# Kernel tuning notes

Measured on AMD Instinct MI355X. Metric: run time of the kernel, lower is better.

## Reference

```python
import jax, jax.numpy as jnp
import numpy as np

L, D, H, E, EH, K = 3, 1024, 16, 8, 256, 2
HD = D // H
B, S, DIN, NOUT = 2, 1024, 32, 8
BASE = 10000.0
EPS = 1e-5


def _ln(x, g, b):
    m = jnp.mean(x, -1, keepdims=True)
    v = jnp.mean((x - m) ** 2, -1, keepdims=True)
    return (x - m) * jax.lax.rsqrt(v + EPS) * g + b


def _rope_tables():
    inv = 1.0 / (BASE ** (jnp.arange(0, HD, 2, dtype=jnp.float32) / HD))
    f = jnp.arange(S, dtype=jnp.float32)[:, None] * inv[None, :]  # [S, HD/2]
    emb = jnp.concatenate([f, f], -1)  # [S, HD]
    return jnp.cos(emb), jnp.sin(emb)


def _rot_half(x):
    x1, x2 = jnp.split(x, 2, axis=-1)
    return jnp.concatenate([-x2, x1], -1)


def setup_inputs() -> dict:
    key = jax.random.key(0)
    ks = iter(jax.random.split(key, 40))
    n = lambda shp, s=0.02: jax.random.normal(next(ks), shp, jnp.float32) * s
    return dict(
        x=jax.random.normal(next(ks), (B, S, DIN), jnp.float32),
        ln1_g=jnp.ones((L, D)), ln1_b=jnp.zeros((L, D)),
        qw=n((L, D, D)), qb=jnp.zeros((L, D)),
        kw=n((L, D, D)), kb=jnp.zeros((L, D)),
        vw=n((L, D, D)), vb=jnp.zeros((L, D)),
        ow=n((L, D, D)), ob=jnp.zeros((L, D)),
        ln2_g=jnp.ones((L, D)), ln2_b=jnp.zeros((L, D)),
        sel_w=n((L, D, E)),
        w1=n((L, E, D, EH)), w2=n((L, E, EH, D)),
        lnf_t_g=jnp.ones((D,)), lnf_t_b=jnp.zeros((D,)),
        lnf_d_g=jnp.ones((D,)), lnf_d_b=jnp.zeros((D,)),
        in_w=n((D, DIN)), in_b=jnp.zeros((D,)),
        out_w=n((NOUT, D)), out_b=jnp.zeros((NOUT,)),
    )


def reference(x, ln1_g, ln1_b, qw, qb, kw, kb, vw, vb, ow, ob, ln2_g, ln2_b,
              sel_w, w1, w2, lnf_t_g, lnf_t_b, lnf_d_g, lnf_d_b,
              in_w, in_b, out_w, out_b):
    cos, sin = _rope_tables()
    scale = HD ** -0.5
    # input projection (torch Linear: x @ W.T + b)
    h = jnp.einsum('bti,di->btd', x, in_w) + in_b

    def layer(h, p):
        l1g, l1b, qw_, qb_, kw_, kb_, vw_, vb_, ow_, ob_, l2g, l2b, selw, w1_, w2_ = p
        xn = _ln(h, l1g, l1b)
        # torch uses F.linear(x, W.t()) => y = x @ W
        def heads(y):
            return y.reshape(B, S, H, HD).transpose(0, 2, 1, 3)
        q = heads(xn @ qw_ + qb_)
        k = heads(xn @ kw_ + kb_)
        v = heads(xn @ vw_ + vb_)
        q = q * cos + _rot_half(q) * sin
        k = k * cos + _rot_half(k) * sin
        attn = jax.nn.softmax(jnp.einsum('bhsd,bhtd->bhst', q, k) * scale, axis=-1)
        o = jnp.einsum('bhst,bhtd->bhsd', attn, v).transpose(0, 2, 1, 3).reshape(B, S, D)
        h = h + jnp.einsum('bsd,od->bso', o, ow_) + ob_
        # SigmaMoE: sigmoid gate, top-k experts, relu FFN experts
        xn = _ln(h, l2g, l2b)
        gates = jax.nn.sigmoid(xn @ selw)  # [B,S,E]
        topv, topi = jax.lax.top_k(gates, K)
        m = jnp.sum(jax.nn.one_hot(topi, E, dtype=xn.dtype) * topv[..., None], axis=-2)  # [B,S,E]
        mid = jax.nn.relu(jnp.einsum('bsd,edh->bseh', xn, w1_))
        moe = jnp.einsum('bseh,ehd->bsd', mid * m[..., None], w2_)
        return h + moe, None

    params = (ln1_g, ln1_b, qw, qb, kw, kb, vw, vb, ow, ob, ln2_g, ln2_b, sel_w, w1, w2)
    h, _ = jax.lax.scan(layer, h, params)
    h = _ln(h, lnf_t_g, lnf_t_b)           # transformer final LN
    last = _ln(h[:, -1, :], lnf_d_g, lnf_d_b)  # decoder LN on last token
    return last @ out_w.T + out_b  # [B, NOUT]
```

## Files before the change

### kernel.cpp

```cpp
#include <hip/hip_runtime.h>


#define LNUM 3
#define D 1024
#define H 16
#define HD 64
#define E 8
#define EH 256
#define B 2
#define S 1024
#define DIN 32
#define NOUT 8
#define EPS 1e-5f
#define TOK (B * S)

typedef __bf16 bf16x8 __attribute__((ext_vector_type(8)));
typedef __bf16 bf16x4 __attribute__((ext_vector_type(4)));
typedef float fx4 __attribute__((ext_vector_type(4)));

__device__ inline float block_reduce_sum256(float v, float* scratch) {
  int lane = threadIdx.x & 63, wv = threadIdx.x >> 6;
#pragma unroll
  for (int off = 32; off; off >>= 1) v += __shfl_down(v, off);
  __syncthreads();
  if (lane == 0) scratch[wv] = v;
  __syncthreads();
  return scratch[0] + scratch[1] + scratch[2] + scratch[3];
}

__global__ __launch_bounds__(256) void ln_bf_kernel(
    const float* __restrict__ in, const float* __restrict__ g,
    const float* __restrict__ bta, __bf16* __restrict__ outb) {
  int token = blockIdx.x;
  int tid = threadIdx.x;
  const float* p = in + (size_t)token * D;
  __shared__ float scratch[4];
  float x[4];
  float s = 0.f, sq = 0.f;
#pragma unroll
  for (int i = 0; i < 4; i++) {
    x[i] = p[tid + i * 256];
    s += x[i];
    sq += x[i] * x[i];
  }
  s = block_reduce_sum256(s, scratch);
  sq = block_reduce_sum256(sq, scratch);
  float mean = s * (1.f / D);
  float inv = rsqrtf(sq * (1.f / D) - mean * mean + EPS);
  __bf16* obp = outb + (size_t)token * D;
#pragma unroll
  for (int i = 0; i < 4; i++) {
    int d = tid + i * 256;
    obp[d] = (__bf16)((x[i] - mean) * inv * g[d] + bta[d]);
  }
}

__global__ __launch_bounds__(256) void ln_gate_kernel(
    const float* __restrict__ in, const float* __restrict__ g,
    const float* __restrict__ bta, const float* __restrict__ selw,
    __bf16* __restrict__ outb, float* __restrict__ gm) {
  int token = blockIdx.x;
  int tid = threadIdx.x;
  const float* p = in + (size_t)token * D;
  __shared__ float scratch[4];
  float x[4];
  float s = 0.f, sq = 0.f;
#pragma unroll
  for (int i = 0; i < 4; i++) {
    x[i] = p[tid + i * 256];
    s += x[i];
    sq += x[i] * x[i];
  }
  s = block_reduce_sum256(s, scratch);
  sq = block_reduce_sum256(sq, scratch);
  float mean = s * (1.f / D);
  float inv = rsqrtf(sq * (1.f / D) - mean * mean + EPS);
  __bf16* obp = outb + (size_t)token * D;
  float ge[E];
#pragma unroll
  for (int e = 0; e < E; e++) ge[e] = 0.f;
#pragma unroll
  for (int i = 0; i < 4; i++) {
    int d = tid + i * 256;
    float y = (x[i] - mean) * inv * g[d] + bta[d];
    obp[d] = (__bf16)y;
#pragma unroll
    for (int e = 0; e < E; e++) ge[e] += y * selw[d * E + e];
  }
  __shared__ float red[4][E];
  int lane = tid & 63, wv = tid >> 6;
#pragma unroll
  for (int e = 0; e < E; e++) {
    float vv = ge[e];
#pragma unroll
    for (int off = 32; off; off >>= 1) vv += __shfl_down(vv, off);
    if (lane == 0) red[wv][e] = vv;
  }
  __syncthreads();
  if (tid == 0) {
    float gg[E];
    for (int e = 0; e < E; e++) {
      float sv = red[0][e] + red[1][e] + red[2][e] + red[3][e];
      gg[e] = 1.f / (1.f + __expf(-sv));
    }
    int i0 = 0;
    for (int e = 1; e < E; e++)
      if (gg[e] > gg[i0]) i0 = e;
    int i1 = -1;
    for (int e = 0; e < E; e++) {
      if (e == i0) continue;
      if (i1 < 0 || gg[e] > gg[i1]) i1 = e;
    }
    float mm[E];
    for (int e = 0; e < E; e++) mm[e] = 0.f;
    mm[i0] = gg[i0];
    mm[i1] = gg[i1];
    for (int e = 0; e < E; e++) gm[(size_t)token * E + e] = mm[e];
  }
}

#define BM 64
#define BKT 16
__global__ __launch_bounds__(256) void gemm_kernel(
    const float* __restrict__ A, const float* __restrict__ Bw,
    const float* __restrict__ bias, float* __restrict__ C, int M, int N,
    int Kd) {
  __shared__ float As[BKT][BM + 1];
  __shared__ float Bs[BKT][BM + 1];
  int bm = blockIdx.y * BM, bn = blockIdx.x * BM;
  int tid = threadIdx.x;
  int tx = tid & 15, ty = tid >> 4;
  float acc[4][4] = {};
  for (int k0 = 0; k0 < Kd; k0 += BKT) {
#pragma unroll
    for (int j = 0; j < 4; j++) {
      int i = tid + j * 256;
      int r = i >> 4, c = i & 15;
      As[c][r] = A[(size_t)(bm + r) * Kd + k0 + c];
    }
#pragma unroll
    for (int j = 0; j < 4; j++) {
      int i = tid + j * 256;
      int n = i >> 4, c = i & 15;
      Bs[c][n] = Bw[(size_t)(bn + n) * Kd + k0 + c];
    }
    __syncthreads();
#pragma unroll
    for (int kk = 0; kk < BKT; kk++) {
      float a[4], bb[4];
#pragma unroll
      for (int i2 = 0; i2 < 4; i2++) a[i2] = As[kk][ty * 4 + i2];
#pragma unroll
      for (int i2 = 0; i2 < 4; i2++) bb[i2] = Bs[kk][tx * 4 + i2];
#pragma unroll
      for (int i2 = 0; i2 < 4; i2++)
#pragma unroll
        for (int j2 = 0; j2 < 4; j2++) acc[i2][j2] += a[i2] * bb[j2];
    }
    __syncthreads();
  }
#pragma unroll
  for (int i2 = 0; i2 < 4; i2++) {
    int row = bm + ty * 4 + i2;
#pragma unroll
    for (int j2 = 0; j2 < 4; j2++) {
      int col = bn + tx * 4 + j2;
      C[(size_t)row * N + col] = acc[i2][j2] + bias[col];
    }
  }
}

template <int NI>
__global__ __launch_bounds__(256) void mfma_gemm(
    const __bf16* __restrict__ A, int lda, const __bf16* __restrict__ Bt,
    const float* __restrict__ bias, float* __restrict__ C,
    __bf16* __restrict__ Cbf, int ldc, __bf16* __restrict__ vT,
    const float* __restrict__ gateScale, int K, int accum, int relu,
    int rope) {
  constexpr int BN = NI * 32;
  __shared__ __bf16 As[2][64 * 32];
  __shared__ __bf16 Bs[2][BN * 32];
  int nwg = gridDim.x * gridDim.y;
  int bid = blockIdx.y * gridDim.x + blockIdx.x;
  int t = (bid & 7) * (nwg >> 3) + (bid >> 3);
  int bxx = t % gridDim.x, byy = t / gridDim.x;
  int bm = byy * 64, bn = bxx * BN;
  int tid = threadIdx.x, lane = tid & 63, wv = tid >> 6;
  int wr = wv >> 1, wc = wv & 1;
  int half = lane >> 4, mrow = lane & 15;
  const __bf16* Ab = A + (size_t)bm * lda;
  const __bf16* Bb = Bt + (size_t)bn * K;
  fx4 acc[2][NI] = {};
  int aslot[2], bslot[NI];
#pragma unroll
  for (int i = 0; i < 2; i++) {
    int row = wr * 32 + i * 16 + mrow;
    aslot[i] = row * 4 + (half ^ ((row >> 1) & 3));
  }
#pragma unroll
  for (int j = 0; j < NI; j++) {
    int row = wc * (NI * 16) + j * 16 + mrow;
    bslot[j] = row * 4 + (half ^ ((row >> 1) & 3));
  }
  int rowa = tid >> 2, kca = (((tid & 3) ^ ((rowa >> 1) & 3)) << 3);

  auto stage = [&](int buf, int k0) {
    __builtin_amdgcn_global_load_lds(
        (const __attribute__((address_space(1))) void*)(Ab +
                                                        (size_t)rowa * lda +
                                                        k0 + kca),
        (__attribute__((address_space(3))) void*)(&As[buf][tid * 8]), 16, 0, 0);
#pragma unroll
    for (int it = 0; it < NI / 2; it++) {
      int c = tid + it * 256;
      int row = c >> 2;
      int kc = (((c & 3) ^ ((row >> 1) & 3)) << 3);
      __builtin_amdgcn_global_load_lds(
          (const __attribute__((address_space(1))) void*)(Bb + (size_t)row * K +
                                                          k0 + kc),
          (__attribute__((address_space(3))) void*)(&Bs[buf][c * 8]), 16, 0, 0);
    }
  };
  stage(0, 0);
  for (int k0 = 0; k0 < K; k0 += 32) {
    int cur = (k0 >> 5) & 1;
    __syncthreads();
    if (k0 + 32 < K) stage(cur ^ 1, k0 + 32);
    bf16x8 af[2], bfr[NI];
#pragma unroll
    for (int i = 0; i < 2; i++)
      af[i] = *(const bf16x8*)(&As[cur][aslot[i] * 8]);
#pragma unroll
    for (int j = 0; j < NI; j++)
      bfr[j] = *(const bf16x8*)(&Bs[cur][bslot[j] * 8]);
#pragma unroll
    for (int i = 0; i < 2; i++)
#pragma unroll
      for (int j = 0; j < NI; j++)
        acc[i][j] = __builtin_amdgcn_mfma_f32_16x16x32_bf16(af[i], bfr[j],
                                                            acc[i][j], 0, 0, 0);
  }
  if (vT && bn >= 2048) {
#pragma unroll
    for (int i = 0; i < 2; i++) {
      int row0 = bm + wr * 32 + i * 16 + half * 4;
#pragma unroll
      for (int j = 0; j < NI; j++) {
        int col = bn + wc * (NI * 16) + j * 16 + mrow;
        float bb = bias ? bias[col] : 0.f;
        bf16x4 pk;
#pragma unroll
        for (int r = 0; r < 4; r++) pk[r] = (__bf16)(acc[i][j][r] + bb);
        *(bf16x4*)(vT + (size_t)(col - 2048) * TOK + row0) = pk;
      }
    }
    return;
  }
#pragma unroll
  for (int i = 0; i < 2; i++) {
#pragma unroll
    for (int r = 0; r < 4; r++) {
      int row = bm + wr * 32 + i * 16 + half * 4 + r;
      float vv[NI];
#pragma unroll
      for (int j = 0; j < NI; j++) {
        int col = bn + wc * (NI * 16) + j * 16 + mrow;
        float val = acc[i][j][r];
        if (bias) val += bias[col];
        if (relu) val = fmaxf(val, 0.f);
        if (gateScale) val *= gateScale[(size_t)row * E + (col >> 8)];
        vv[j] = val;
      }
      if (rope && NI == 4) {
        int spos = row & (S - 1);
#pragma unroll
        for (int jj = 0; jj < 2; jj++) {
          int hd = jj * 16 + mrow;
          float invf = exp2f(hd * -0.4152410118609825f);
          float ang = (float)spos * invf;
          float sn, cs;
          __sincosf(ang, &sn, &cs);
          float a0 = vv[jj], a1 = vv[jj + 2];
          vv[jj] = a0 * cs - a1 * sn;
          vv[jj + 2] = a1 * cs + a0 * sn;
        }
      }
#pragma unroll
      for (int j = 0; j < NI; j++) {
        int col = bn + wc * (NI * 16) + j * 16 + mrow;
        size_t addr = (size_t)row * ldc + col;
        if (Cbf)
          Cbf[addr] = (__bf16)vv[j];
        else if (accum)
          C[addr] += vv[j];
        else
          C[addr] = vv[j];
      }
    }
  }
}

__global__ void transpose_cvt(const float* __restrict__ src, long long srcZ,
                              __bf16* __restrict__ dst, int zmod,
                              long long dstZa, long long dstZb, int R, int C,
                              int dstLd) {
  __shared__ float t[32][33];
  int r0 = blockIdx.y * 32, c0 = blockIdx.x * 32;
  int z = blockIdx.z;
  src += (size_t)z * srcZ;
  dst += (size_t)(z / zmod) * dstZb + (size_t)(z % zmod) * dstZa;
  int tx = threadIdx.x, ty = threadIdx.y;
#pragma unroll
  for (int i = 0; i < 4; i++) {
    int r = r0 + ty + i * 8;
    t[ty + i * 8][tx] = src[(size_t)r * C + c0 + tx];
  }
  __syncthreads();
#pragma unroll
  for (int i = 0; i < 4; i++) {
    int c = c0 + ty + i * 8;
    dst[(size_t)c * dstLd + r0 + tx] = (__bf16)t[tx][ty + i * 8];
  }
}

__global__ void cvt_kernel(const float* __restrict__ s, __bf16* __restrict__ d,
                           int n) {
  for (int i = blockIdx.x * 256 + threadIdx.x; i < n; i += gridDim.x * 256)
    d[i] = (__bf16)s[i];
}

__global__ void bias_all(const float* __restrict__ a,
                         const float* __restrict__ b,
                         const float* __restrict__ c, float* __restrict__ dst) {
  int i = blockIdx.x * 256 + threadIdx.x;
  if (i >= LNUM * 3 * D) return;
  int l = i / (3 * D), r = i % (3 * D);
  int w = r / D, d = r % D;
  const float* src = w == 0 ? a : (w == 1 ? b : c);
  dst[i] = src[l * D + d];
}

#define P_LD 72
__global__ __launch_bounds__(256) void attn_dbuf(
    const __bf16* __restrict__ qk, const __bf16* __restrict__ vT,
    __bf16* __restrict__ obf) {
  __shared__ __bf16 Kt[2][64 * 64];
  __shared__ __bf16 Vt[2][64 * 64];
  __shared__ __bf16 Pb[4][16 * P_LD];
  int nwg = gridDim.x * gridDim.y;
  int bid = blockIdx.y * gridDim.x + blockIdx.x;
  int t = (bid & 7) * (nwg >> 3) + (bid >> 3);
  int hb = t / gridDim.y;
  int q0 = (t % gridDim.y) * 64;
  int hh = hb >> 1, b = hb & 1;
  int tid = threadIdx.x, lane = tid & 63, wv = tid >> 6;
  int col = lane & 15, half = lane >> 4;
  const float scale = 0.125f;
  __bf16* P = &Pb[wv][0];

  const __bf16* qp = qk + (size_t)(b * S + q0 + wv * 16 + col) * 2048 + hh * HD;
  bf16x8 qf0 = *(const bf16x8*)(qp + half * 8);
  bf16x8 qf1 = *(const bf16x8*)(qp + 32 + half * 8);
  const __bf16* kbase = qk + (size_t)(b * S) * 2048 + 1024 + hh * HD;
  const __bf16* vbase = vT + (size_t)(hh * HD) * TOK + b * S;

  int srow = tid >> 3, sslot = tid & 7;
  int sg = sslot ^ (srow & 7);
  int srow2 = (tid + 256) >> 3, sslot2 = tid & 7;
  int sg2 = sslot2 ^ (srow2 & 7);

  auto stage = [&](int buf, int t0) {
    __builtin_amdgcn_global_load_lds(
        (const __attribute__((address_space(1))) void*)(kbase +
                                                        (size_t)(t0 + srow) *
                                                            2048 +
                                                        sg * 8),
        (__attribute__((address_space(3))) void*)(&Kt[buf][tid * 8]), 16, 0, 0);
    __builtin_amdgcn_global_load_lds(
        (const __attribute__((address_space(1))) void*)(kbase +
                                                        (size_t)(t0 + srow2) *
                                                            2048 +
                                                        sg2 * 8),
        (__attribute__((address_space(3))) void*)(&Kt[buf][(tid + 256) * 8]),
        16, 0, 0);
    __builtin_amdgcn_global_load_lds(
        (const __attribute__((address_space(1))) void*)(vbase +
                                                        (size_t)srow * TOK +
                                                        t0 + sg * 8),
        (__attribute__((address_space(3))) void*)(&Vt[buf][tid * 8]), 16, 0, 0);
    __builtin_amdgcn_global_load_lds(
        (const __attribute__((address_space(1))) void*)(vbase +
                                                        (size_t)srow2 * TOK +
                                                        t0 + sg2 * 8),
        (__attribute__((address_space(3))) void*)(&Vt[buf][(tid + 256) * 8]),
        16, 0, 0);
  };

  fx4 Oacc[4] = {};
  float lpart[4] = {0.f, 0.f, 0.f, 0.f};

  stage(0, 0);
  for (int t0 = 0; t0 < S; t0 += 64) {
    int cur = (t0 >> 6) & 1;
    __syncthreads();
    if (t0 + 64 < S) stage(cur ^ 1, t0 + 64);
    fx4 sacc[4] = {};
#pragma unroll
    for (int n = 0; n < 4; n++) {
      int rowk = n * 16 + col;
      const __bf16* kp = &Kt[cur][rowk * 64];
      bf16x8 b0 = *(const bf16x8*)(kp + ((half ^ (rowk & 7)) << 3));
      bf16x8 b1 = *(const bf16x8*)(kp + (((4 + half) ^ (rowk & 7)) << 3));
      sacc[n] =
          __builtin_amdgcn_mfma_f32_16x16x32_bf16(qf0, b0, sacc[n], 0, 0, 0);
      sacc[n] =
          __builtin_amdgcn_mfma_f32_16x16x32_bf16(qf1, b1, sacc[n], 0, 0, 0);
    }
#pragma unroll
    for (int r = 0; r < 4; r++) {
      int prow = (half * 4 + r) * P_LD;
#pragma unroll
      for (int n = 0; n < 4; n++) {
        float p = __expf(sacc[n][r] * scale);
        lpart[r] += p;
        P[prow + n * 16 + col] = (__bf16)p;
      }
    }
#pragma unroll
    for (int k0 = 0; k0 < 2; k0++) {
      bf16x8 af = *(const bf16x8*)(P + col * P_LD + k0 * 32 + half * 8);
#pragma unroll
      for (int n = 0; n < 4; n++) {
        int rowd = n * 16 + col;
        int g = k0 * 4 + half;
        bf16x8 bv =
            *(const bf16x8*)(&Vt[cur][rowd * 64 + ((g ^ (rowd & 7)) << 3)]);
        Oacc[n] =
            __builtin_amdgcn_mfma_f32_16x16x32_bf16(af, bv, Oacc[n], 0, 0, 0);
      }
    }
  }
#pragma unroll
  for (int r = 0; r < 4; r++) {
    float l = lpart[r];
#pragma unroll
    for (int msk = 1; msk < 16; msk <<= 1) l += __shfl_xor(l, msk);
    float inv = 1.f / l;
    int row = q0 + wv * 16 + half * 4 + r;
    __bf16* op = obf + (size_t)(b * S + row) * D + hh * HD;
#pragma unroll
    for (int n = 0; n < 4; n++) op[n * 16 + col] = (__bf16)(Oacc[n][r] * inv);
  }
}

__global__ __launch_bounds__(256) void final_kernel(
    const float* __restrict__ h, const float* __restrict__ tg,
    const float* __restrict__ tb, const float* __restrict__ dg,
    const float* __restrict__ db, const float* __restrict__ ow,
    const float* __restrict__ ob, float* __restrict__ out) {
  int b = blockIdx.x;
  int tid = threadIdx.x;
  __shared__ float scratch[4];
  __shared__ float yf[D];
  const float* p = h + ((size_t)(b * S + (S - 1))) * D;
  float x[4];
  float s = 0.f, sq = 0.f;
#pragma unroll
  for (int i = 0; i < 4; i++) {
    x[i] = p[tid + i * 256];
    s += x[i];
    sq += x[i] * x[i];
  }
  s = block_reduce_sum256(s, scratch);
  sq = block_reduce_sum256(sq, scratch);
  float mean = s * (1.f / D);
  float inv = rsqrtf(sq * (1.f / D) - mean * mean + EPS);
  float y[4];
  s = 0.f;
  sq = 0.f;
#pragma unroll
  for (int i = 0; i < 4; i++) {
    int d = tid + i * 256;
    y[i] = (x[i] - mean) * inv * tg[d] + tb[d];
    s += y[i];
    sq += y[i] * y[i];
  }
  s = block_reduce_sum256(s, scratch);
  sq = block_reduce_sum256(sq, scratch);
  float mean2 = s * (1.f / D);
  float inv2 = rsqrtf(sq * (1.f / D) - mean2 * mean2 + EPS);
#pragma unroll
  for (int i = 0; i < 4; i++) {
    int d = tid + i * 256;
    yf[d] = (y[i] - mean2) * inv2 * dg[d] + db[d];
  }
  __syncthreads();
  for (int oo = 0; oo < NOUT; oo++) {
    float part = 0.f;
    for (int d = tid; d < D; d += 256) part += yf[d] * ow[(size_t)oo * D + d];
    part = block_reduce_sum256(part, scratch);
    if (tid == 0) out[b * NOUT + oo] = part + ob[oo];
  }
}

extern "C" void kernel_launch(void* const* d_in, const int* in_sizes, int n_in,
                              void* d_out, int out_size, void* d_ws,
                              size_t ws_size, hipStream_t stream) {
  const float* x = (const float*)d_in[0];
  const float* ln1_g = (const float*)d_in[1];
  const float* ln1_b = (const float*)d_in[2];
  const float* qw = (const float*)d_in[3];
  const float* qb_ = (const float*)d_in[4];
  const float* kw = (const float*)d_in[5];
  const float* kb_ = (const float*)d_in[6];
  const float* vw = (const float*)d_in[7];
  const float* vb_ = (const float*)d_in[8];
  const float* ow = (const float*)d_in[9];
  const float* ob = (const float*)d_in[10];
  const float* ln2_g = (const float*)d_in[11];
  const float* ln2_b = (const float*)d_in[12];
  const float* selw = (const float*)d_in[13];
  const float* w1 = (const float*)d_in[14];
  const float* w2 = (const float*)d_in[15];
  const float* lntg = (const float*)d_in[16];
  const float* lntb = (const float*)d_in[17];
  const float* lndg = (const float*)d_in[18];
  const float* lndb = (const float*)d_in[19];
  const float* inw = (const float*)d_in[20];
  const float* inb = (const float*)d_in[21];
  const float* outw = (const float*)d_in[22];
  const float* outb = (const float*)d_in[23];
  float* out = (float*)d_out;

  float* h = (float*)d_ws;
  float* gm = h + (size_t)TOK * D;
  float* qkvbias = gm + (size_t)TOK * E;
  __bf16* xnb = (__bf16*)(qkvbias + LNUM * 3 * D);
  __bf16* qkbf = xnb + (size_t)TOK * D;
  __bf16* vTb = qkbf + (size_t)TOK * 2048;
  __bf16* obf = vTb + (size_t)D * TOK;
  __bf16* qkvt = obf + (size_t)TOK * D;
  __bf16* owt = qkvt + (size_t)LNUM * 3 * D * D;
  __bf16* w1t = owt + (size_t)LNUM * D * D;
  __bf16* w2t = w1t + (size_t)LNUM * E * EH * D;
  __bf16* midb = qkbf;

  transpose_cvt<<<dim3(32, 32, LNUM), dim3(32, 8), 0, stream>>>(
      qw, (long long)D * D, qkvt, 1024, (long long)3 * D * D, 0, D, D, D);
  transpose_cvt<<<dim3(32, 32, LNUM), dim3(32, 8), 0, stream>>>(
      kw, (long long)D * D, qkvt + (size_t)D * D, 1024, (long long)3 * D * D, 0,
      D, D, D);
  transpose_cvt<<<dim3(32, 32, LNUM), dim3(32, 8), 0, stream>>>(
      vw, (long long)D * D, qkvt + (size_t)2 * D * D, 1024,
      (long long)3 * D * D, 0, D, D, D);
  cvt_kernel<<<1024, 256, 0, stream>>>(ow, owt, LNUM * D * D);
  transpose_cvt<<<dim3(EH / 32, D / 32, LNUM * E), dim3(32, 8), 0, stream>>>(
      w1, (long long)D * EH, w1t, 1024, (long long)EH * D, 0, D, EH, D);
  transpose_cvt<<<dim3(D / 32, EH / 32, LNUM * E), dim3(32, 8), 0, stream>>>(
      w2, (long long)EH * D, w2t, E, EH, (long long)D * E * EH, EH, D, E * EH);
  bias_all<<<(LNUM * 3 * D + 255) / 256, 256, 0, stream>>>(qb_, kb_, vb_,
                                                           qkvbias);

  gemm_kernel<<<dim3(D / 64, TOK / 64), 256, 0, stream>>>(x, inw, inb, h, TOK,
                                                          D, DIN);
  for (int l = 0; l < LNUM; l++) {
    ln_bf_kernel<<<TOK, 256, 0, stream>>>(h, ln1_g + l * D, ln1_b + l * D, xnb);
    mfma_gemm<4><<<dim3(3072 / 128, TOK / 64), 256, 0, stream>>>(
        xnb, D, qkvt + (size_t)l * 3 * D * D, qkvbias + l * 3 * D, nullptr,
        qkbf, 2048, vTb, nullptr, D, 0, 0, 1);
    attn_dbuf<<<dim3(H * B, S / 64), 256, 0, stream>>>(qkbf, vTb, obf);
    mfma_gemm<2><<<dim3(D / 64, TOK / 64), 256, 0, stream>>>(
        obf, D, owt + (size_t)l * D * D, ob + l * D, h, nullptr, D, nullptr,
        nullptr, D, 1, 0, 0);
    ln_gate_kernel<<<TOK, 256, 0, stream>>>(h, ln2_g + l * D, ln2_b + l * D,
                                            selw + (size_t)l * D * E, xnb, gm);
    mfma_gemm<4><<<dim3(2048 / 128, TOK / 64), 256, 0, stream>>>(
        xnb, D, w1t + (size_t)l * E * EH * D, nullptr, nullptr, midb, 2048,
        nullptr, gm, D, 0, 1, 0);
    mfma_gemm<2><<<dim3(D / 64, TOK / 64), 256, 0, stream>>>(
        midb, 2048, w2t + (size_t)l * D * E * EH, nullptr, h, nullptr, D,
        nullptr, nullptr, 2048, 1, 0, 0);
  }
  final_kernel<<<B, 256, 0, stream>>>(h, lntg, lntb, lndg, lndb, outw, outb,
                                      out);
}
```

Measured before the change: 631.3 us.

## Route MoE second projection through per-expert token lists with atomic scatter

The gate kernel now appends each token to per-expert index lists using atomic counters. A new grouped kernel computes the second expert matmul only for the tokens routed to each expert and scatter-adds the results into the residual with float atomics. This skips the dense product over all eight experts for every token, trading it for gathered loads, atomic adds on the output and nondeterministic summation order. The first expert projection still runs densely for all experts.

```diff
diff --git a/kernel.cpp b/kernel.cpp
--- a/kernel.cpp
+++ b/kernel.cpp
@@ -58,7 +58,8 @@
 __global__ __launch_bounds__(256) void ln_gate_kernel(
     const float* __restrict__ in, const float* __restrict__ g,
     const float* __restrict__ bta, const float* __restrict__ selw,
-    __bf16* __restrict__ outb, float* __restrict__ gm) {
+    __bf16* __restrict__ outb, float* __restrict__ gm, int* __restrict__ idx,
+    int* __restrict__ cnt) {
   int token = blockIdx.x;
   int tid = threadIdx.x;
   const float* p = in + (size_t)token * D;
@@ -116,6 +117,10 @@
     mm[i0] = gg[i0];
     mm[i1] = gg[i1];
     for (int e = 0; e < E; e++) gm[(size_t)token * E + e] = mm[e];
+    int p0 = atomicAdd(&cnt[i0], 1);
+    idx[i0 * TOK + p0] = token;
+    int p1 = atomicAdd(&cnt[i1], 1);
+    idx[i1 * TOK + p1] = token;
   }
 }
 
@@ -300,6 +305,94 @@
   }
 }
 
+__global__ __launch_bounds__(256) void moe_w2(
+    const __bf16* __restrict__ midb, const __bf16* __restrict__ w2t,
+    float* __restrict__ hout, const int* __restrict__ idx,
+    const int* __restrict__ cnt) {
+  int e = blockIdx.y >> 5, mt = blockIdx.y & 31;
+  int cnt_e = cnt[e];
+  int ent0 = mt * 64;
+  if (ent0 >= cnt_e) return;
+  int nc = blockIdx.x;
+  __shared__ __bf16 As[2][64 * 32];
+  __shared__ __bf16 Bs[2][128 * 32];
+  int tid = threadIdx.x, lane = tid & 63, wv = tid >> 6;
+  int wr = wv >> 1, wc = wv & 1;
+  int half = lane >> 4, mrow = lane & 15;
+  const int* idx_e = idx + e * TOK;
+
+  int rowa = tid >> 2, kca = (((tid & 3) ^ ((rowa >> 1) & 3)) << 3);
+  int entA = ent0 + rowa;
+  int tokA = entA < cnt_e ? idx_e[entA] : 0;
+  const __bf16* Arow = midb + (size_t)tokA * 2048 + e * EH;
+  const __bf16* Bb = w2t + (size_t)(nc * 128) * (E * EH) + e * EH;
+
+  fx4 acc[2][4] = {};
+  int aslot[2], bslot[4];
+#pragma unroll
+  for (int i = 0; i < 2; i++) {
+    int row = wr * 32 + i * 16 + mrow;
+    aslot[i] = row * 4 + (half ^ ((row >> 1) & 3));
+  }
+#pragma unroll
+  for (int j = 0; j < 4; j++) {
+    int row = wc * 64 + j * 16 + mrow;
+    bslot[j] = row * 4 + (half ^ ((row >> 1) & 3));
+  }
+
+  auto stage = [&](int buf, int k0) {
+    __builtin_amdgcn_global_load_lds(
+        (const __attribute__((address_space(1))) void*)(Arow + k0 + kca),
+        (__attribute__((address_space(3))) void*)(&As[buf][tid * 8]), 16, 0, 0);
+#pragma unroll
+    for (int it = 0; it < 2; it++) {
+      int c = tid + it * 256;
+      int row = c >> 2;
+      int kc = (((c & 3) ^ ((row >> 1) & 3)) << 3);
+      __builtin_amdgcn_global_load_lds(
+          (const __attribute__((address_space(1))) void*)(Bb +
+                                                          (size_t)row *
+                                                              (E * EH) +
+                                                          k0 + kc),
+          (__attribute__((address_space(3))) void*)(&Bs[buf][c * 8]), 16, 0, 0);
+    }
+  };
+  stage(0, 0);
+  for (int k0 = 0; k0 < EH; k0 += 32) {
+    int cur = (k0 >> 5) & 1;
+    __syncthreads();
+    if (k0 + 32 < EH) stage(cur ^ 1, k0 + 32);
+    bf16x8 af[2], bfr[4];
+#pragma unroll
+    for (int i = 0; i < 2; i++)
+      af[i] = *(const bf16x8*)(&As[cur][aslot[i] * 8]);
+#pragma unroll
+    for (int j = 0; j < 4; j++)
+      bfr[j] = *(const bf16x8*)(&Bs[cur][bslot[j] * 8]);
+#pragma unroll
+    for (int i = 0; i < 2; i++)
+#pragma unroll
+      for (int j = 0; j < 4; j++)
+        acc[i][j] = __builtin_amdgcn_mfma_f32_16x16x32_bf16(af[i], bfr[j],
+                                                            acc[i][j], 0, 0, 0);
+  }
+#pragma unroll
+  for (int i = 0; i < 2; i++) {
+#pragma unroll
+    for (int r = 0; r < 4; r++) {
+      int ent = ent0 + wr * 32 + i * 16 + half * 4 + r;
+      if (ent < cnt_e) {
+        int tok = idx_e[ent];
+#pragma unroll
+        for (int j = 0; j < 4; j++) {
+          int col = nc * 128 + wc * 64 + j * 16 + mrow;
+          unsafeAtomicAdd(&hout[(size_t)tok * D + col], acc[i][j][r]);
+        }
+      }
+    }
+  }
+}
+
 __global__ void transpose_cvt(const float* __restrict__ src, long long srcZ,
                               __bf16* __restrict__ dst, int zmod,
                               long long dstZa, long long dstZb, int R, int C,
@@ -331,8 +424,10 @@
 
 __global__ void bias_all(const float* __restrict__ a,
                          const float* __restrict__ b,
-                         const float* __restrict__ c, float* __restrict__ dst) {
+                         const float* __restrict__ c, float* __restrict__ dst,
+                         int* __restrict__ cnt) {
   int i = blockIdx.x * 256 + threadIdx.x;
+  if (i < LNUM * E) cnt[i] = 0;
   if (i >= LNUM * 3 * D) return;
   int l = i / (3 * D), r = i % (3 * D);
   int w = r / D, d = r % D;
@@ -543,6 +638,8 @@
   __bf16* owt = qkvt + (size_t)LNUM * 3 * D * D;
   __bf16* w1t = owt + (size_t)LNUM * D * D;
   __bf16* w2t = w1t + (size_t)LNUM * E * EH * D;
+  int* moeIdx = (int*)(w2t + (size_t)LNUM * D * E * EH);
+  int* moeCnt = moeIdx + (size_t)E * TOK;
   __bf16* midb = qkbf;
 
   transpose_cvt<<<dim3(32, 32, LNUM), dim3(32, 8), 0, stream>>>(
@@ -559,7 +656,7 @@
   transpose_cvt<<<dim3(D / 32, EH / 32, LNUM * E), dim3(32, 8), 0, stream>>>(
       w2, (long long)EH * D, w2t, E, EH, (long long)D * E * EH, EH, D, E * EH);
   bias_all<<<(LNUM * 3 * D + 255) / 256, 256, 0, stream>>>(qb_, kb_, vb_,
-                                                           qkvbias);
+                                                           qkvbias, moeCnt);
 
   gemm_kernel<<<dim3(D / 64, TOK / 64), 256, 0, stream>>>(x, inw, inb, h, TOK,
                                                           D, DIN);
@@ -573,13 +670,13 @@
         obf, D, owt + (size_t)l * D * D, ob + l * D, h, nullptr, D, nullptr,
         nullptr, D, 1, 0, 0);
     ln_gate_kernel<<<TOK, 256, 0, stream>>>(h, ln2_g + l * D, ln2_b + l * D,
-                                            selw + (size_t)l * D * E, xnb, gm);
+                                            selw + (size_t)l * D * E, xnb, gm,
+                                            moeIdx, moeCnt + l * E);
     mfma_gemm<4><<<dim3(2048 / 128, TOK / 64), 256, 0, stream>>>(
         xnb, D, w1t + (size_t)l * E * EH * D, nullptr, nullptr, midb, 2048,
         nullptr, gm, D, 0, 1, 0);
-    mfma_gemm<2><<<dim3(D / 64, TOK / 64), 256, 0, stream>>>(
-        midb, 2048, w2t + (size_t)l * D * E * EH, nullptr, h, nullptr, D,
-        nullptr, nullptr, 2048, 1, 0, 0);
+    moe_w2<<<dim3(8, E * 32), 256, 0, stream>>>(
+        midb, w2t + (size_t)l * D * E * EH, h, moeIdx, moeCnt + l * E);
   }
   final_kernel<<<B, 256, 0, stream>>>(h, lntg, lntb, lndg, lndb, outw, outb,
                                       out);
```

Result: slower. 734.7 us (+16.4%).
